# Kernel tuning notes

Hardware: AMD Instinct MI355X
Metric: run time of the kernel (lower is better)

## Reference

```python
import jax, jax.numpy as jnp
import numpy as np

B = 512          # batch of visual features
VF_D = 4096      # visual feature dim (VGG fc7)
HID_D = 2048     # hidden dim
EMB_D = 300      # order-embedding / label-vector dim
N_LABELS = 2000  # number of GT label vectors


def setup_inputs() -> dict:
    key = jax.random.key(0)
    ks = jax.random.split(key, 4)
    vfs = jax.random.normal(ks[0], (B, VF_D), dtype=jnp.float32)
    W1 = jax.random.normal(ks[1], (VF_D, HID_D), dtype=jnp.float32) * (1.0 / np.sqrt(VF_D))
    b1 = jnp.zeros((HID_D,), dtype=jnp.float32)
    W2 = jax.random.normal(ks[2], (HID_D, EMB_D), dtype=jnp.float32) * (1.0 / np.sqrt(HID_D))
    b2 = jnp.zeros((EMB_D,), dtype=jnp.float32)
    gt_label_vecs = jax.random.normal(ks[3], (N_LABELS, EMB_D), dtype=jnp.float32)
    return {"vfs": vfs, "W1": W1, "b1": b1, "W2": W2, "b2": b2,
            "gt_label_vecs": gt_label_vecs}


def reference(vfs, W1, b1, W2, b2, gt_label_vecs):
    # hidden_layer: ReLU -> (Dropout, identity at eval) -> Linear
    vf_hidden = jnp.dot(jax.nn.relu(vfs), W1) + b1            # [B, HID_D]
    # embedding_layer: ReLU -> Linear
    vf_emb = jnp.dot(jax.nn.relu(vf_hidden), W2) + b2         # [B, EMB_D]
    # order_sim(hypers=gt_label_vecs, hypos=vf_emb):
    #   score = -|| clamp(hypo - hyper, min=0) ||^2, batched over all pairs
    diff = jax.nn.relu(vf_emb[:, None, :] - gt_label_vecs[None, :, :])  # [B, N, D]
    score_stack = -jnp.sum(diff * diff, axis=-1)              # [B, N_LABELS]
    return score_stack, vf_emb
```

## Files before the change

kernel.cpp:

```cpp
#include <hip/hip_runtime.h>

#define B_SZ   512
#define VFD    4096
#define HIDD   2048
#define EMBD   300
#define NLAB   2000
#define NPAD   320

#define G1_SPLIT 4
#define G2_SPLIT 8
#define SD_SPLIT 4

typedef __attribute__((ext_vector_type(8))) short short8x;
typedef __attribute__((ext_vector_type(4))) float f32x4;
typedef __attribute__((ext_vector_type(8))) unsigned short ushort8;
typedef __attribute__((ext_vector_type(4))) unsigned short ushort4x;

typedef const __attribute__((address_space(1))) unsigned int* gas_t;
typedef __attribute__((address_space(3))) unsigned int* las_t;

__device__ inline unsigned short f2bf(float x) {
    unsigned u = __float_as_uint(x);
    u += 0x7FFF + ((u >> 16) & 1);
    return (unsigned short)(u >> 16);
}

__global__ __launch_bounds__(256) void prep_kernel(
    const float* __restrict__ vfs, unsigned short* __restrict__ Xb,
    const float* __restrict__ W1, unsigned short* __restrict__ W1T,
    const float* __restrict__ W2, unsigned short* __restrict__ W2T)
{
    __shared__ float tile[64][65];
    const int tid = threadIdx.x;
    const int blk = blockIdx.x;

    if (blk < 1024) {
        const int i = (blk * 256 + tid) * 8;
        float4 a = *(const float4*)&vfs[i];
        float4 b = *(const float4*)&vfs[i + 4];
        ushort8 o;
        o[0] = f2bf(fmaxf(a.x, 0.f)); o[1] = f2bf(fmaxf(a.y, 0.f));
        o[2] = f2bf(fmaxf(a.z, 0.f)); o[3] = f2bf(fmaxf(a.w, 0.f));
        o[4] = f2bf(fmaxf(b.x, 0.f)); o[5] = f2bf(fmaxf(b.y, 0.f));
        o[6] = f2bf(fmaxf(b.z, 0.f)); o[7] = f2bf(fmaxf(b.w, 0.f));
        *(ushort8*)&Xb[i] = o;
        return;
    }

    const float* in; unsigned short* out; int N, ldK, bx, by;
    if (blk < 3072) {
        const int b = blk - 1024;
        in = W1; out = W1T; N = HIDD; ldK = VFD; bx = b & 31; by = b >> 5;
    } else {
        const int b = blk - 3072;
        in = W2; out = W2T; N = EMBD; ldK = HIDD; bx = b % 5; by = b / 5;
    }
    const int n0 = bx * 64, k0 = by * 64;

    #pragma unroll
    for (int i = 0; i < 4; ++i) {
        const int s = tid + 256 * i;
        const int kr = s >> 4, nc = (s & 15) * 4;
        float4 v = {0.f, 0.f, 0.f, 0.f};
        if (n0 + nc < N) v = *(const float4*)&in[(size_t)(k0 + kr) * N + n0 + nc];
        tile[kr][nc + 0] = v.x; tile[kr][nc + 1] = v.y;
        tile[kr][nc + 2] = v.z; tile[kr][nc + 3] = v.w;
    }
    __syncthreads();

    const int row = tid >> 2, kq = (tid & 3) * 16;
    ushort8 o0, o1;
    #pragma unroll
    for (int j = 0; j < 8; ++j) o0[j] = f2bf(tile[kq + j][row]);
    #pragma unroll
    for (int j = 0; j < 8; ++j) o1[j] = f2bf(tile[kq + 8 + j][row]);
    const size_t off = (size_t)(n0 + row) * ldK + k0 + kq;
    *(ushort8*)&out[off]     = o0;
    *(ushort8*)&out[off + 8] = o1;
}

template<int LDA, int LDB, int LDC, int KCHUNK>
__global__ __launch_bounds__(256) void gemm_bf16_kernel(
    const unsigned short* __restrict__ A,
    const unsigned short* __restrict__ Bt,
    float* __restrict__ Cpart, int M)
{
    __shared__ unsigned short As[2][2048];
    __shared__ unsigned short Bs[2][2048];

    const int tid = threadIdx.x;
    const int m0 = blockIdx.y * 64, n0 = blockIdx.x * 64;
    const int kbase = blockIdx.z * KCHUNK;

    const int soct = tid >> 6, srow = tid & 63;
    const unsigned short* ga = A  + (size_t)(m0 + srow) * LDA + kbase + soct * 8;
    const unsigned short* gb = Bt + (size_t)(n0 + srow) * LDB + kbase + soct * 8;

    const int lane = tid & 63;
    const int wave = tid >> 6;
    const int wm = (wave & 1) * 32;
    const int wn = (wave >> 1) * 32;
    const int q = lane >> 4, l15 = lane & 15;

    f32x4 acc00 = {0.f,0.f,0.f,0.f}, acc01 = {0.f,0.f,0.f,0.f};
    f32x4 acc10 = {0.f,0.f,0.f,0.f}, acc11 = {0.f,0.f,0.f,0.f};

    __builtin_amdgcn_global_load_lds((gas_t)(const void*)ga,
                                     (las_t)(void*)&As[0][tid * 8], 16, 0, 0);
    __builtin_amdgcn_global_load_lds((gas_t)(const void*)gb,
                                     (las_t)(void*)&Bs[0][tid * 8], 16, 0, 0);

    const int iters = KCHUNK / 32;
    for (int t = 0; t < iters; ++t) {
        const int cur = t & 1, nxt = cur ^ 1;
        __syncthreads();

        if (t + 1 < iters) {
            __builtin_amdgcn_global_load_lds((gas_t)(const void*)(ga + (t + 1) * 32),
                                             (las_t)(void*)&As[nxt][tid * 8], 16, 0, 0);
            __builtin_amdgcn_global_load_lds((gas_t)(const void*)(gb + (t + 1) * 32),
                                             (las_t)(void*)&Bs[nxt][tid * 8], 16, 0, 0);
        }

        short8x a0 = *(short8x*)&As[cur][(q * 64 + wm +      l15) * 8];
        short8x a1 = *(short8x*)&As[cur][(q * 64 + wm + 16 + l15) * 8];
        short8x b0 = *(short8x*)&Bs[cur][(q * 64 + wn +      l15) * 8];
        short8x b1 = *(short8x*)&Bs[cur][(q * 64 + wn + 16 + l15) * 8];
        acc00 = __builtin_amdgcn_mfma_f32_16x16x32_bf16(a0, b0, acc00, 0, 0, 0);
        acc01 = __builtin_amdgcn_mfma_f32_16x16x32_bf16(a0, b1, acc01, 0, 0, 0);
        acc10 = __builtin_amdgcn_mfma_f32_16x16x32_bf16(a1, b0, acc10, 0, 0, 0);
        acc11 = __builtin_amdgcn_mfma_f32_16x16x32_bf16(a1, b1, acc11, 0, 0, 0);
    }

    float* Cz = Cpart + (size_t)blockIdx.z * M * LDC;
    #pragma unroll
    for (int r = 0; r < 4; ++r) {
        const int rr = m0 + wm + q * 4 + r;
        const int cc = n0 + wn + l15;
        Cz[(size_t)rr * LDC + cc]             = acc00[r];
        Cz[(size_t)rr * LDC + cc + 16]        = acc01[r];
        Cz[(size_t)(rr + 16) * LDC + cc]      = acc10[r];
        Cz[(size_t)(rr + 16) * LDC + cc + 16] = acc11[r];
    }
}

__global__ __launch_bounds__(256) void reduce_h_kernel(
    const float* __restrict__ Hpart, const float* __restrict__ b1,
    unsigned short* __restrict__ Hb)
{
    const int i = (blockIdx.x * 256 + threadIdx.x) * 4;
    const int col = i & (HIDD - 1);
    float4 s = *(const float4*)&b1[col];
    #pragma unroll
    for (int z = 0; z < G1_SPLIT; ++z) {
        float4 p = *(const float4*)&Hpart[(size_t)z * B_SZ * HIDD + i];
        s.x += p.x; s.y += p.y; s.z += p.z; s.w += p.w;
    }
    ushort4x o;
    o[0] = f2bf(fmaxf(s.x, 0.f));
    o[1] = f2bf(fmaxf(s.y, 0.f));
    o[2] = f2bf(fmaxf(s.z, 0.f));
    o[3] = f2bf(fmaxf(s.w, 0.f));
    *(ushort4x*)&Hb[i] = o;
}

__global__ __launch_bounds__(256) void reduce_e_kernel(
    const float* __restrict__ Epart, const float* __restrict__ b2,
    float* __restrict__ E)
{
    const int gid = blockIdx.x * 256 + threadIdx.x;
    if (gid >= B_SZ * EMBD) return;
    const int m = gid / EMBD, n = gid - m * EMBD;
    float v = b2[n];
    #pragma unroll
    for (int z = 0; z < G2_SPLIT; ++z)
        v += Epart[(size_t)z * B_SZ * NPAD + m * NPAD + n];
    E[gid] = v;
}

__global__ __launch_bounds__(128) void scores_part_kernel(
    const float* __restrict__ E, const float* __restrict__ G,
    float* __restrict__ part)
{
    __shared__ float Gs[64][44];

    const int tid = threadIdx.x;
    const int tx = tid & 15, ty = tid >> 4;
    const int n0 = blockIdx.x * 64, b0 = blockIdx.y * 32;
    const int dbase = blockIdx.z * (NPAD / SD_SPLIT);

    float acc[4][4] = {};

    for (int dc = 0; dc < NPAD / SD_SPLIT; dc += 40) {
        const int d0 = dbase + dc;
        __syncthreads();
        #pragma unroll
        for (int i = 0; i < 5; ++i) {
            const int s = tid + 128 * i;
            const int row = s / 10, qd = (s - row * 10) * 4;
            const int d = d0 + qd;
            const int n = n0 + row;
            float4 v = {0.f, 0.f, 0.f, 0.f};
            if (n < NLAB && d < EMBD) v = *(const float4*)&G[(size_t)n * EMBD + d];
            *(float4*)&Gs[row][qd] = v;
        }
        __syncthreads();

        #pragma unroll 2
        for (int d = 0; d < 40; d += 4) {
            const int dd = d0 + d;
            float4 e[4];
            if (dd < EMBD) {
                #pragma unroll
                for (int r = 0; r < 4; ++r)
                    e[r] = *(const float4*)&E[(size_t)(b0 + ty * 4 + r) * EMBD + dd];
            } else {
                #pragma unroll
                for (int r = 0; r < 4; ++r) e[r] = make_float4(0.f, 0.f, 0.f, 0.f);
            }
            #pragma unroll
            for (int c = 0; c < 4; ++c) {
                float4 g = *(float4*)&Gs[tx + 16 * c][d];
                #pragma unroll
                for (int r = 0; r < 4; ++r) {
                    float t;
                    t = fmaxf(e[r].x - g.x, 0.f); acc[r][c] += t * t;
                    t = fmaxf(e[r].y - g.y, 0.f); acc[r][c] += t * t;
                    t = fmaxf(e[r].z - g.z, 0.f); acc[r][c] += t * t;
                    t = fmaxf(e[r].w - g.w, 0.f); acc[r][c] += t * t;
                }
            }
        }
    }

    float* pz = part + (size_t)blockIdx.z * B_SZ * NLAB;
    #pragma unroll
    for (int r = 0; r < 4; ++r) {
        const int b = b0 + ty * 4 + r;
        #pragma unroll
        for (int c = 0; c < 4; ++c) {
            const int n = n0 + tx + 16 * c;
            if (n < NLAB) pz[(size_t)b * NLAB + n] = acc[r][c];
        }
    }
}

__global__ __launch_bounds__(256) void scores_combine_kernel(
    const float* __restrict__ part, float* __restrict__ scores)
{
    const int i = (blockIdx.x * 256 + threadIdx.x) * 4;
    float4 s = {0.f, 0.f, 0.f, 0.f};
    #pragma unroll
    for (int z = 0; z < SD_SPLIT; ++z) {
        float4 p = *(const float4*)&part[(size_t)z * B_SZ * NLAB + i];
        s.x += p.x; s.y += p.y; s.z += p.z; s.w += p.w;
    }
    float4 o = make_float4(-s.x, -s.y, -s.z, -s.w);
    *(float4*)&scores[i] = o;
}

extern "C" void kernel_launch(void* const* d_in, const int* in_sizes, int n_in,
                              void* d_out, int out_size, void* d_ws, size_t ws_size,
                              hipStream_t stream)
{
    const float* vfs = (const float*)d_in[0];
    const float* W1  = (const float*)d_in[1];
    const float* b1  = (const float*)d_in[2];
    const float* W2  = (const float*)d_in[3];
    const float* b2  = (const float*)d_in[4];
    const float* G   = (const float*)d_in[5];

    float* out    = (float*)d_out;
    float* scores = out;
    float* E      = out + (size_t)B_SZ * NLAB;

    char* ws = (char*)d_ws;
    unsigned short* Xb  = (unsigned short*)(ws);
    unsigned short* W1T = (unsigned short*)(ws + 4194304);
    unsigned short* W2T = (unsigned short*)(ws + 20971520);
    unsigned short* Hb  = (unsigned short*)(ws + 22282240);
    float*          Hpart = (float*)(ws + 24379392);
    float*          Epart = (float*)(ws + 41156608);
    float*          Spart = (float*)(ws + 24379392);

    prep_kernel<<<3232, 256, 0, stream>>>(vfs, Xb, W1, W1T, W2, W2T);

    gemm_bf16_kernel<VFD, VFD, HIDD, VFD / G1_SPLIT>
        <<<dim3(32, 8, G1_SPLIT), 256, 0, stream>>>(Xb, W1T, Hpart, B_SZ);
    reduce_h_kernel<<<1024, 256, 0, stream>>>(Hpart, b1, Hb);

    gemm_bf16_kernel<HIDD, HIDD, NPAD, HIDD / G2_SPLIT>
        <<<dim3(5, 8, G2_SPLIT), 256, 0, stream>>>(Hb, W2T, Epart, B_SZ);
    reduce_e_kernel<<<600, 256, 0, stream>>>(Epart, b2, E);

    scores_part_kernel<<<dim3(32, 16, SD_SPLIT), 128, 0, stream>>>(E, G, Spart);
    scores_combine_kernel<<<1000, 256, 0, stream>>>(Spart, scores);
}
```

Measured before the change: 178.2 us.

## Widen GEMM1 tile to 64x128 and replace score split-reduce with atomics

```diff
diff --git a/kernel.cpp b/kernel.cpp
--- a/kernel.cpp
+++ b/kernel.cpp
@@ -79,6 +79,80 @@
     *(ushort8*)&out[off + 8] = o1;
 }
 
+__global__ __launch_bounds__(256) void gemm1_kernel(
+    const unsigned short* __restrict__ A,
+    const unsigned short* __restrict__ Bt,
+    float* __restrict__ Cpart)
+{
+    __shared__ unsigned short As[2][2048];
+    __shared__ unsigned short Bs[2][4096];
+
+    const int tid = threadIdx.x;
+    const int m0 = blockIdx.y * 64, n0 = blockIdx.x * 128;
+    const int kbase = blockIdx.z * (VFD / G1_SPLIT);
+
+    const unsigned short* ga = A + (size_t)(m0 + (tid & 63)) * VFD + kbase + (tid >> 6) * 8;
+    const int brow = tid & 127, boct = tid >> 7;
+    const unsigned short* gb0 = Bt + (size_t)(n0 + brow) * VFD + kbase + boct * 8;
+    const unsigned short* gb1 = gb0 + 16;
+
+    const int lane = tid & 63;
+    const int wave = tid >> 6;
+    const int wm = (wave & 1) * 32;
+    const int wn = (wave >> 1) * 64;
+    const int q = lane >> 4, l15 = lane & 15;
+
+    f32x4 acc[2][4];
+    #pragma unroll
+    for (int r = 0; r < 2; ++r)
+        #pragma unroll
+        for (int c = 0; c < 4; ++c) acc[r][c] = (f32x4){0.f,0.f,0.f,0.f};
+
+    __builtin_amdgcn_global_load_lds((gas_t)(const void*)ga,
+                                     (las_t)(void*)&As[0][tid * 8], 16, 0, 0);
+    __builtin_amdgcn_global_load_lds((gas_t)(const void*)gb0,
+                                     (las_t)(void*)&Bs[0][tid * 8], 16, 0, 0);
+    __builtin_amdgcn_global_load_lds((gas_t)(const void*)gb1,
+                                     (las_t)(void*)&Bs[0][(tid + 256) * 8], 16, 0, 0);
+
+    const int iters = (VFD / G1_SPLIT) / 32;
+    for (int t = 0; t < iters; ++t) {
+        const int cur = t & 1, nxt = cur ^ 1;
+        __syncthreads();
+
+        if (t + 1 < iters) {
+            const int ko = (t + 1) * 32;
+            __builtin_amdgcn_global_load_lds((gas_t)(const void*)(ga + ko),
+                                             (las_t)(void*)&As[nxt][tid * 8], 16, 0, 0);
+            __builtin_amdgcn_global_load_lds((gas_t)(const void*)(gb0 + ko),
+                                             (las_t)(void*)&Bs[nxt][tid * 8], 16, 0, 0);
+            __builtin_amdgcn_global_load_lds((gas_t)(const void*)(gb1 + ko),
+                                             (las_t)(void*)&Bs[nxt][(tid + 256) * 8], 16, 0, 0);
+        }
+
+        short8x a0 = *(short8x*)&As[cur][(q * 64 + wm +      l15) * 8];
+        short8x a1 = *(short8x*)&As[cur][(q * 64 + wm + 16 + l15) * 8];
+        #pragma unroll
+        for (int c = 0; c < 4; ++c) {
+            short8x b = *(short8x*)&Bs[cur][(q * 128 + wn + c * 16 + l15) * 8];
+            acc[0][c] = __builtin_amdgcn_mfma_f32_16x16x32_bf16(a0, b, acc[0][c], 0, 0, 0);
+            acc[1][c] = __builtin_amdgcn_mfma_f32_16x16x32_bf16(a1, b, acc[1][c], 0, 0, 0);
+        }
+    }
+
+    float* Cz = Cpart + (size_t)blockIdx.z * B_SZ * HIDD;
+    #pragma unroll
+    for (int r = 0; r < 2; ++r) {
+        #pragma unroll
+        for (int g = 0; g < 4; ++g) {
+            const int rr = m0 + wm + r * 16 + q * 4 + g;
+            #pragma unroll
+            for (int c = 0; c < 4; ++c)
+                Cz[(size_t)rr * HIDD + n0 + wn + c * 16 + l15] = acc[r][c][g];
+        }
+    }
+}
+
 template<int LDA, int LDB, int LDC, int KCHUNK>
 __global__ __launch_bounds__(256) void gemm_bf16_kernel(
     const unsigned short* __restrict__ A,
@@ -92,9 +166,8 @@
     const int m0 = blockIdx.y * 64, n0 = blockIdx.x * 64;
     const int kbase = blockIdx.z * KCHUNK;
 
-    const int soct = tid >> 6, srow = tid & 63;
-    const unsigned short* ga = A  + (size_t)(m0 + srow) * LDA + kbase + soct * 8;
-    const unsigned short* gb = Bt + (size_t)(n0 + srow) * LDB + kbase + soct * 8;
+    const unsigned short* ga = A  + (size_t)(m0 + (tid & 63)) * LDA + kbase + (tid >> 6) * 8;
+    const unsigned short* gb = Bt + (size_t)(n0 + (tid & 63)) * LDB + kbase + (tid >> 6) * 8;
 
     const int lane = tid & 63;
     const int wave = tid >> 6;
@@ -164,23 +237,32 @@
     *(ushort4x*)&Hb[i] = o;
 }
 
-__global__ __launch_bounds__(256) void reduce_e_kernel(
+__global__ __launch_bounds__(256) void reduce_e_zero_kernel(
     const float* __restrict__ Epart, const float* __restrict__ b2,
-    float* __restrict__ E)
-{
-    const int gid = blockIdx.x * 256 + threadIdx.x;
-    if (gid >= B_SZ * EMBD) return;
-    const int m = gid / EMBD, n = gid - m * EMBD;
-    float v = b2[n];
-    #pragma unroll
-    for (int z = 0; z < G2_SPLIT; ++z)
-        v += Epart[(size_t)z * B_SZ * NPAD + m * NPAD + n];
-    E[gid] = v;
+    float* __restrict__ E, float* __restrict__ scores)
+{
+    const int blk = blockIdx.x;
+    if (blk < 600) {
+        const int gid = blk * 256 + threadIdx.x;
+        if (gid >= B_SZ * EMBD) return;
+        const int m = gid / EMBD, n = gid - m * EMBD;
+        float v = b2[n];
+        #pragma unroll
+        for (int z = 0; z < G2_SPLIT; ++z)
+            v += Epart[(size_t)z * B_SZ * NPAD + m * NPAD + n];
+        E[gid] = v;
+    } else {
+        const int i = ((blk - 600) * 256 + threadIdx.x) * 4;
+        if (i < B_SZ * NLAB) {
+            float4 z = {0.f, 0.f, 0.f, 0.f};
+            *(float4*)&scores[i] = z;
+        }
+    }
 }
 
 __global__ __launch_bounds__(128) void scores_part_kernel(
     const float* __restrict__ E, const float* __restrict__ G,
-    float* __restrict__ part)
+    float* __restrict__ scores)
 {
     __shared__ float Gs[64][44];
 
@@ -233,30 +315,15 @@
         }
     }
 
-    float* pz = part + (size_t)blockIdx.z * B_SZ * NLAB;
     #pragma unroll
     for (int r = 0; r < 4; ++r) {
         const int b = b0 + ty * 4 + r;
         #pragma unroll
         for (int c = 0; c < 4; ++c) {
             const int n = n0 + tx + 16 * c;
-            if (n < NLAB) pz[(size_t)b * NLAB + n] = acc[r][c];
-        }
-    }
-}
-
-__global__ __launch_bounds__(256) void scores_combine_kernel(
-    const float* __restrict__ part, float* __restrict__ scores)
-{
-    const int i = (blockIdx.x * 256 + threadIdx.x) * 4;
-    float4 s = {0.f, 0.f, 0.f, 0.f};
-    #pragma unroll
-    for (int z = 0; z < SD_SPLIT; ++z) {
-        float4 p = *(const float4*)&part[(size_t)z * B_SZ * NLAB + i];
-        s.x += p.x; s.y += p.y; s.z += p.z; s.w += p.w;
-    }
-    float4 o = make_float4(-s.x, -s.y, -s.z, -s.w);
-    *(float4*)&scores[i] = o;
+            if (n < NLAB) atomicAdd(&scores[(size_t)b * NLAB + n], -acc[r][c]);
+        }
+    }
 }
 
 extern "C" void kernel_launch(void* const* d_in, const int* in_sizes, int n_in,
@@ -281,18 +348,15 @@
     unsigned short* Hb  = (unsigned short*)(ws + 22282240);
     float*          Hpart = (float*)(ws + 24379392);
     float*          Epart = (float*)(ws + 41156608);
-    float*          Spart = (float*)(ws + 24379392);
 
     prep_kernel<<<3232, 256, 0, stream>>>(vfs, Xb, W1, W1T, W2, W2T);
 
-    gemm_bf16_kernel<VFD, VFD, HIDD, VFD / G1_SPLIT>
-        <<<dim3(32, 8, G1_SPLIT), 256, 0, stream>>>(Xb, W1T, Hpart, B_SZ);
+    gemm1_kernel<<<dim3(16, 8, G1_SPLIT), 256, 0, stream>>>(Xb, W1T, Hpart);
     reduce_h_kernel<<<1024, 256, 0, stream>>>(Hpart, b1, Hb);
 
     gemm_bf16_kernel<HIDD, HIDD, NPAD, HIDD / G2_SPLIT>
         <<<dim3(5, 8, G2_SPLIT), 256, 0, stream>>>(Hb, W2T, Epart, B_SZ);
-    reduce_e_kernel<<<600, 256, 0, stream>>>(Epart, b2, E);
-
-    scores_part_kernel<<<dim3(32, 16, SD_SPLIT), 128, 0, stream>>>(E, G, Spart);
-    scores_combine_kernel<<<1000, 256, 0, stream>>>(Spart, scores);
-}
+    reduce_e_zero_kernel<<<1624, 256, 0, stream>>>(Epart, b2, E, scores);
+
+    scores_part_kernel<<<dim3(32, 16, SD_SPLIT), 128, 0, stream>>>(E, G, scores);
+}
```

Result: faster. 174.5 us (-2.1%).
